# Kernel optimization log

Hardware: AMD Instinct MI355X
Metric: run time of the kernel (lower is better)

Reference implementation:

```python
import jax, jax.numpy as jnp
import numpy as np

DIM = 1024
NUM_HEADS = 16
HEAD_DIM = DIM // NUM_HEADS
EPS = 1e-6


def setup_inputs() -> dict:
    key = jax.random.key(0)
    ks = jax.random.split(key, 9)
    B, S = 4, 4096
    std = 1.0 / np.sqrt(DIM)
    inp = {
        "x": jax.random.normal(ks[0], (B, S, DIM), dtype=jnp.float32),
        "attention_mask": jnp.ones((B, S), dtype=jnp.float32),
        "Wq": jax.random.normal(ks[1], (DIM, DIM), dtype=jnp.float32) * std,
        "bq": jnp.zeros((DIM,), dtype=jnp.float32),
        "Wk": jax.random.normal(ks[2], (DIM, DIM), dtype=jnp.float32) * std,
        "bk": jnp.zeros((DIM,), dtype=jnp.float32),
        "Wv": jax.random.normal(ks[3], (DIM, DIM), dtype=jnp.float32) * std,
        "bv": jnp.zeros((DIM,), dtype=jnp.float32),
        "Wo": jax.random.normal(ks[4], (DIM, DIM), dtype=jnp.float32) * std,
        "bo": jnp.zeros((DIM,), dtype=jnp.float32),
    }
    return inp


def _phi(x):
    # ELU + 1 feature map (positive-valued kernel features)
    return jax.nn.elu(x) + 1.0


def reference(x, attention_mask, Wq, bq, Wk, bk, Wv, bv, Wo, bo):
    B, S, _ = x.shape
    H, D = NUM_HEADS, HEAD_DIM
    q = (x @ Wq.T + bq).reshape(B, S, H, D)
    k = (x @ Wk.T + bk).reshape(B, S, H, D)
    v = (x @ Wv.T + bv).reshape(B, S, H, D)
    q = _phi(q)
    k = _phi(k)
    m = attention_mask[:, :, None, None]
    k = k * m
    v = v * m
    # kv state: [B, H, D, D]
    kv = jnp.einsum("bshd,bshm->bhdm", k, v)
    qkv = jnp.einsum("bshd,bhdm->bshm", q, kv)
    k_sum = k.sum(axis=1)  # [B, H, D]
    normalizer = jnp.einsum("bshd,bhd->bsh", q, k_sum) + EPS
    out = (qkv / normalizer[..., None]).reshape(B, S, DIM)
    return out @ Wo.T + bo
```

## Files before the change

### kernel.cpp

```cpp
#include <hip/hip_runtime.h>

typedef unsigned short u16;
typedef float f32x4 __attribute__((ext_vector_type(4)));
typedef __bf16 bf16x8 __attribute__((ext_vector_type(8)));
typedef unsigned short us8 __attribute__((ext_vector_type(8)));

#define EPS_ 1e-6f

__device__ __forceinline__ u16 f2bf(float f) {
    unsigned u = __float_as_uint(f);
    u += 0x7FFFu + ((u >> 16) & 1u);
    return (u16)(u >> 16);
}
__device__ __forceinline__ float bf2f(u16 h) {
    return __uint_as_float(((unsigned)h) << 16);
}
__device__ __forceinline__ void gload_lds16(const void* g, void* l) {
    __builtin_amdgcn_global_load_lds(
        (const __attribute__((address_space(1))) void*)g,
        (__attribute__((address_space(3))) void*)l, 16, 0, 0);
}

__global__ __launch_bounds__(256) void f32_to_bf16_kernel(
    const float* __restrict__ src, u16* __restrict__ dst, int n4)
{
    int i = blockIdx.x * 256 + threadIdx.x;
    if (i >= n4) return;
    float4 f = ((const float4*)src)[i];
    ushort4 o;
    o.x = f2bf(f.x); o.y = f2bf(f.y); o.z = f2bf(f.z); o.w = f2bf(f.w);
    ((ushort4*)dst)[i] = o;
}


__device__ __forceinline__ void stage_half(
    const u16* __restrict__ src, int K, int kbase, char* slot, int tid)
{
    const int w = tid >> 6, l = tid & 63;
    #pragma unroll
    for (int j = 0; j < 2; ++j) {
        int c16 = j * 512 + w * 64 + l;
        int row = c16 >> 2;
        int sl  = c16 & 3;
        int ksrc = kbase + ((sl ^ ((row >> 1) & 3)) << 3);
        gload_lds16(src + (size_t)row * K + ksrc, slot + j * 8192 + w * 1024);
    }
}

#define BARRIER()  asm volatile("s_barrier" ::: "memory")
#define VMCNT8()   asm volatile("s_waitcnt vmcnt(8)" ::: "memory")
#define LGKM0()    asm volatile("s_waitcnt lgkmcnt(0)" ::: "memory")

#define LOADA(base, MOFF) \
    af0 = *(const bf16x8*)((base) + aoff + (MOFF) + 0);    \
    af1 = *(const bf16x8*)((base) + aoff + (MOFF) + 1024); \
    af2 = *(const bf16x8*)((base) + aoff + (MOFF) + 2048); \
    af3 = *(const bf16x8*)((base) + aoff + (MOFF) + 3072);

#define LOADB(base) \
    bf0 = *(const bf16x8*)((base) + boff + 0);    \
    bf1 = *(const bf16x8*)((base) + boff + 1024); \
    bf2 = *(const bf16x8*)((base) + boff + 2048); \
    bf3 = *(const bf16x8*)((base) + boff + 3072);

#define MFMA1(M_, N_, AF_, BF_) \
    acc[M_][N_] = __builtin_amdgcn_mfma_f32_16x16x32_bf16(BF_, AF_, acc[M_][N_], 0, 0, 0)

#define MFMA_BLOCK(M0) do { \
    MFMA1(M0+0, 0, af0, bf0); MFMA1(M0+0, 1, af0, bf1); MFMA1(M0+0, 2, af0, bf2); MFMA1(M0+0, 3, af0, bf3); \
    MFMA1(M0+1, 0, af1, bf0); MFMA1(M0+1, 1, af1, bf1); MFMA1(M0+1, 2, af1, bf2); MFMA1(M0+1, 3, af1, bf3); \
    MFMA1(M0+2, 0, af2, bf0); MFMA1(M0+2, 1, af2, bf1); MFMA1(M0+2, 2, af2, bf2); MFMA1(M0+2, 3, af2, bf3); \
    MFMA1(M0+3, 0, af3, bf0); MFMA1(M0+3, 1, af3, bf1); MFMA1(M0+3, 2, af3, bf2); MFMA1(M0+3, 3, af3, bf3); \
} while (0)

template<int MODE>
__global__ __launch_bounds__(512, 2) void gemm8p(
    const u16* __restrict__ A, const u16* __restrict__ B,
    const float* __restrict__ bias,
    u16* __restrict__ oq, u16* __restrict__ ok, u16* __restrict__ ov,
    float* __restrict__ outf, int M, int N, int K)
{
    extern __shared__ char lds[];
    const int tid  = threadIdx.x;
    const int lane = tid & 63;
    const int wv   = tid >> 6;
    const int wm   = wv >> 2;
    const int wn   = wv & 3;
    const int NT = K >> 6;

    int bx, by;
    {
        const int gx = gridDim.x;
        int wg  = blockIdx.y * gx + blockIdx.x;
        int cpx = (gx * gridDim.y) >> 3;
        int swz = (wg & 7) * cpx + (wg >> 3);
        bx = swz % gx; by = swz / gx;
    }

    const u16* Ab = A + (size_t)by * 256 * K;
    const u16* Bb = B + (size_t)bx * 256 * K;

    const int i  = lane & 15, g = lane >> 4;
    const int fo = ((g ^ ((i >> 1) & 3)) << 4);
    const int aoff = (wm * 128 + i) * 64 + fo;
    const int boff = (wn * 64 + i) * 64 + fo;

    f32x4 acc[8][4];
    #pragma unroll
    for (int m = 0; m < 8; ++m)
        #pragma unroll
        for (int n = 0; n < 4; ++n) {
            acc[m][n][0] = 0.f; acc[m][n][1] = 0.f;
            acc[m][n][2] = 0.f; acc[m][n][3] = 0.f;
        }

    stage_half(Ab, K, 0,  lds + 0,             tid);
    stage_half(Bb, K, 0,  lds + 16384,         tid);
    stage_half(Ab, K, 32, lds + 32768,         tid);
    stage_half(Bb, K, 32, lds + 49152,         tid);
    stage_half(Ab, K, 64, lds + 65536 + 0,     tid);
    stage_half(Bb, K, 64, lds + 65536 + 16384, tid);
    VMCNT8();
    BARRIER();

    for (int t = 0; t < NT; ++t) {
        char* cb = lds + ((t & 1) << 16);
        char* nb = lds + (((t + 1) & 1) << 16);
        const int t1 = (t + 1 < NT) ? t + 1 : NT - 1;
        const int t2 = (t + 2 < NT) ? t + 2 : NT - 1;
        const int k1src = t1 * 64 + 32;
        const int k2src = t2 * 64;

        bf16x8 af0, af1, af2, af3, bf0, bf1, bf2, bf3;

        LOADA(cb, 0);
        LOADB(cb + 16384);
        stage_half(Ab, K, k1src, nb + 32768, tid);
        BARRIER();
        LGKM0();
        __builtin_amdgcn_s_setprio(1);
        MFMA_BLOCK(0);
        __builtin_amdgcn_s_setprio(0);
        BARRIER();

        LOADA(cb, 4096);
        stage_half(Bb, K, k1src, nb + 49152, tid);
        VMCNT8();
        BARRIER();
        LGKM0();
        __builtin_amdgcn_s_setprio(1);
        MFMA_BLOCK(4);
        __builtin_amdgcn_s_setprio(0);
        BARRIER();

        LOADA(cb + 32768, 0);
        LOADB(cb + 49152);
        stage_half(Ab, K, k2src, cb + 0, tid);
        BARRIER();
        LGKM0();
        __builtin_amdgcn_s_setprio(1);
        MFMA_BLOCK(0);
        __builtin_amdgcn_s_setprio(0);
        BARRIER();

        LOADA(cb + 32768, 4096);
        stage_half(Bb, K, k2src, cb + 16384, tid);
        VMCNT8();
        BARRIER();
        LGKM0();
        __builtin_amdgcn_s_setprio(1);
        MFMA_BLOCK(4);
        __builtin_amdgcn_s_setprio(0);
        BARRIER();
    }
    asm volatile("s_waitcnt vmcnt(0)" ::: "memory");

    const int rowg0 = by * 256 + wm * 128;
    const int colg0 = bx * 256 + wn * 64;

    if (MODE == 1) {
        const int which = colg0 >> 10;
        u16* dst = (which == 0) ? oq : ((which == 1) ? ok : ov);
        const bool dophi = (which < 2);
        const int cbo = colg0 & 1023;
        float4 bs[4];
        #pragma unroll
        for (int n = 0; n < 4; ++n)
            bs[n] = *(const float4*)(bias + colg0 + n * 16 + g * 4);
        #pragma unroll
        for (int m = 0; m < 8; ++m) {
            int row = rowg0 + m * 16 + i;
            #pragma unroll
            for (int n = 0; n < 4; ++n) {
                float v0 = acc[m][n][0] + bs[n].x;
                float v1 = acc[m][n][1] + bs[n].y;
                float v2 = acc[m][n][2] + bs[n].z;
                float v3 = acc[m][n][3] + bs[n].w;
                if (dophi) {
                    v0 = (v0 > 0.f) ? (v0 + 1.f) : __expf(v0);
                    v1 = (v1 > 0.f) ? (v1 + 1.f) : __expf(v1);
                    v2 = (v2 > 0.f) ? (v2 + 1.f) : __expf(v2);
                    v3 = (v3 > 0.f) ? (v3 + 1.f) : __expf(v3);
                }
                ushort4 o;
                o.x = f2bf(v0); o.y = f2bf(v1); o.z = f2bf(v2); o.w = f2bf(v3);
                *(ushort4*)(dst + (size_t)row * 1024 + cbo + n * 16 + g * 4) = o;
            }
        }
    } else {
        float4 bs[4];
        #pragma unroll
        for (int n = 0; n < 4; ++n)
            bs[n] = *(const float4*)(bias + colg0 + n * 16 + g * 4);
        #pragma unroll
        for (int m = 0; m < 8; ++m) {
            int row = rowg0 + m * 16 + i;
            #pragma unroll
            for (int n = 0; n < 4; ++n) {
                float4 o;
                o.x = acc[m][n][0] + bs[n].x;
                o.y = acc[m][n][1] + bs[n].y;
                o.z = acc[m][n][2] + bs[n].z;
                o.w = acc[m][n][3] + bs[n].w;
                *(float4*)(outf + (size_t)row * N + colg0 + n * 16 + g * 4) = o;
            }
        }
    }
}

__global__ __launch_bounds__(256) void kv_partial(
    const u16* __restrict__ kbf, const u16* __restrict__ vbf,
    const float* __restrict__ mask, float* __restrict__ kvp, float* __restrict__ ksp)
{
    const int bh = blockIdx.x, ch = blockIdx.y;
    const int b = bh >> 4, h = bh & 15;
    const int tid = threadIdx.x;
    __shared__ __align__(16) float ks[32][64];
    __shared__ __align__(16) float vs[32][64];
    const int dg = tid >> 4, mg = tid & 15;
    float acc[4][4] = {};
    float ksa[4] = {};
    const int s0 = ch * 256;
    const int lr = tid >> 3, lc = (tid & 7) * 8;
    for (int sb = 0; sb < 256; sb += 32) {
        {
            size_t grow = (size_t)b * 4096 + (s0 + sb + lr);
            float mm = mask[grow];
            size_t off = (grow << 10) + (h << 6) + lc;
            us8 ku = __builtin_bit_cast(us8, *(const bf16x8*)(kbf + off));
            us8 vu = __builtin_bit_cast(us8, *(const bf16x8*)(vbf + off));
            #pragma unroll
            for (int j = 0; j < 8; ++j) {
                ks[lr][lc + j] = bf2f(ku[j]) * mm;
                vs[lr][lc + j] = bf2f(vu[j]) * mm;
            }
        }
        __syncthreads();
        #pragma unroll
        for (int ss = 0; ss < 32; ++ss) {
            float4 k4 = *(const float4*)&ks[ss][dg << 2];
            float4 v4 = *(const float4*)&vs[ss][mg << 2];
            float ka[4] = {k4.x, k4.y, k4.z, k4.w};
            float va[4] = {v4.x, v4.y, v4.z, v4.w};
            #pragma unroll
            for (int di = 0; di < 4; ++di) {
                ksa[di] += ka[di];
                #pragma unroll
                for (int mi = 0; mi < 4; ++mi) acc[di][mi] += ka[di] * va[mi];
            }
        }
        __syncthreads();
    }
    float* o = kvp + (((size_t)ch * 64 + bh) << 12);
    #pragma unroll
    for (int di = 0; di < 4; ++di)
        #pragma unroll
        for (int mi = 0; mi < 4; ++mi)
            o[(dg * 4 + di) * 64 + (mg * 4 + mi)] = acc[di][mi];
    if (mg == 0) {
        float* os = ksp + (((size_t)ch * 64 + bh) << 6);
        #pragma unroll
        for (int di = 0; di < 4; ++di) os[dg * 4 + di] = ksa[di];
    }
}

__global__ __launch_bounds__(256) void kv_reduce(
    const float* __restrict__ kvp, const float* __restrict__ ksp,
    u16* __restrict__ kvTbf, u16* __restrict__ ksumbf)
{
    const int bh = blockIdx.x, tid = threadIdx.x;
    for (int idx = tid; idx < 4096; idx += 256) {
        float s = 0.f;
        #pragma unroll
        for (int c = 0; c < 16; ++c) s += kvp[(((size_t)c * 64 + bh) << 12) + idx];
        int d = idx >> 6, m = idx & 63;
        kvTbf[((size_t)bh << 12) + (m << 6) + d] = f2bf(s);
    }
    if (tid < 64) {
        float s = 0.f;
        #pragma unroll
        for (int c = 0; c < 16; ++c) s += ksp[(((size_t)c * 64 + bh) << 6) + tid];
        ksumbf[(bh << 6) + tid] = f2bf(s);
    }
}

__global__ __launch_bounds__(256) void attn_kernel(
    const u16* __restrict__ qbf, const u16* __restrict__ kvTbf,
    const u16* __restrict__ ksumbf, u16* __restrict__ attnbf)
{
    const int bh = blockIdx.x;
    const int b = bh >> 4, h = bh & 15;
    const int tid = threadIdx.x, lane = tid & 63, wv = tid >> 6;
    __shared__ __align__(16) u16 kvs[64 * 64];
    __shared__ __align__(16) u16 kss[64];

    {
        const uint4* src = (const uint4*)(kvTbf + ((size_t)bh << 12));
        for (int u = tid; u < 512; u += 256) {
            uint4 d4 = src[u];
            int m = u >> 3, slot = u & 7;
            *(uint4*)((char*)kvs + m * 128 + ((slot ^ (m & 7)) << 4)) = d4;
        }
        if (tid < 32)
            ((unsigned*)kss)[tid] = ((const unsigned*)(ksumbf + ((size_t)bh << 6)))[tid];
    }
    __syncthreads();

    bf16x8 bfr[2][4], bnf[2];
    #pragma unroll
    for (int kk = 0; kk < 2; ++kk) {
        int kslot = kk * 4 + (lane >> 4);
        #pragma unroll
        for (int n = 0; n < 4; ++n) {
            int m = n * 16 + (lane & 15);
            bfr[kk][n] = *(const bf16x8*)((const char*)kvs + m * 128 +
                                          ((kslot ^ (m & 7)) << 4));
        }
        #pragma unroll
        for (int i2 = 0; i2 < 8; ++i2) bnf[kk][i2] = (__bf16)0.0f;
        if ((lane & 15) == 0)
            bnf[kk] = *(const bf16x8*)((const char*)kss + (kslot << 4));
    }

    const int sbase = blockIdx.y * 256 + wv * 16;
    for (int it = 0; it < 4; ++it) {
        const int st = sbase + it * 64;
        f32x4 acc[4], nacc;
        #pragma unroll
        for (int n = 0; n < 4; ++n) {
            acc[n][0] = 0.f; acc[n][1] = 0.f; acc[n][2] = 0.f; acc[n][3] = 0.f;
        }
        nacc[0] = 0.f; nacc[1] = 0.f; nacc[2] = 0.f; nacc[3] = 0.f;
        #pragma unroll
        for (int kk = 0; kk < 2; ++kk) {
            size_t goff = (((size_t)(b * 4096 + st + (lane & 15))) << 10) +
                          (h << 6) + kk * 32 + ((lane >> 4) << 3);
            bf16x8 af = *(const bf16x8*)(qbf + goff);
            #pragma unroll
            for (int n = 0; n < 4; ++n)
                acc[n] = __builtin_amdgcn_mfma_f32_16x16x32_bf16(af, bfr[kk][n], acc[n], 0, 0, 0);
            nacc = __builtin_amdgcn_mfma_f32_16x16x32_bf16(af, bnf[kk], nacc, 0, 0, 0);
        }
        float inv[4];
        #pragma unroll
        for (int j = 0; j < 4; ++j) {
            float nj = __shfl(nacc[j], lane & 48);
            inv[j] = 1.0f / (nj + EPS_);
        }
        #pragma unroll
        for (int n = 0; n < 4; ++n)
            #pragma unroll
            for (int j = 0; j < 4; ++j) {
                int row = st + ((lane >> 4) << 2) + j;
                attnbf[(((size_t)(b * 4096 + row)) << 10) + (h << 6) + n * 16 + (lane & 15)]
                    = f2bf(acc[n][j] * inv[j]);
            }
    }
}

extern "C" void kernel_launch(void* const* d_in, const int* in_sizes, int n_in,
                              void* d_out, int out_size, void* d_ws, size_t ws_size,
                              hipStream_t stream) {
    const float* x    = (const float*)d_in[0];
    const float* mask = (const float*)d_in[1];
    const float* Wq   = (const float*)d_in[2];
    const float* bq   = (const float*)d_in[3];
    const float* Wk   = (const float*)d_in[4];
    const float* bk   = (const float*)d_in[5];
    const float* Wv   = (const float*)d_in[6];
    const float* bv   = (const float*)d_in[7];
    const float* Wo   = (const float*)d_in[8];
    const float* bo   = (const float*)d_in[9];
    float* out = (float*)d_out;

    if (ws_size < 142606336u) return;

    char* ws = (char*)d_ws;
    u16*   xbf    = (u16*)ws;
    u16*   wqkvbf = (u16*)(ws + 33554432);
    float* bcat   = (float*)(ws + 39845888);
    u16*   qbf    = (u16*)(ws + 41943040);
    u16*   kbf    = qbf + 16777216;
    u16*   vbf    = kbf + 16777216;
    u16*   attnbf = kbf;
    float* kvp    = (float*)ws;
    float* ksp    = (float*)(ws + 16777216);
    u16*   kvTbf  = (u16*)(ws + 17039360);
    u16*   ksumbf = (u16*)(ws + 17563648);
    u16*   wobf   = (u16*)(ws + 20971520);

    f32_to_bf16_kernel<<<16384, 256, 0, stream>>>(x,  xbf,  16777216 / 4);
    f32_to_bf16_kernel<<<1024,  256, 0, stream>>>(Wq, wqkvbf,           1048576 / 4);
    f32_to_bf16_kernel<<<1024,  256, 0, stream>>>(Wk, wqkvbf + 1048576, 1048576 / 4);
    f32_to_bf16_kernel<<<1024,  256, 0, stream>>>(Wv, wqkvbf + 2097152, 1048576 / 4);
    hipMemcpyAsync(bcat,        bq, 4096, hipMemcpyDeviceToDevice, stream);
    hipMemcpyAsync(bcat + 1024, bk, 4096, hipMemcpyDeviceToDevice, stream);
    hipMemcpyAsync(bcat + 2048, bv, 4096, hipMemcpyDeviceToDevice, stream);

    gemm8p<1><<<dim3(12, 64), 512, 131072, stream>>>(
        xbf, wqkvbf, bcat, qbf, kbf, vbf, nullptr, 16384, 3072, 1024);

    f32_to_bf16_kernel<<<1024, 256, 0, stream>>>(Wo, wobf, 1048576 / 4);

    kv_partial<<<dim3(64, 16), 256, 0, stream>>>(kbf, vbf, mask, kvp, ksp);
    kv_reduce<<<64, 256, 0, stream>>>(kvp, ksp, kvTbf, ksumbf);

    attn_kernel<<<dim3(64, 16), 256, 0, stream>>>(qbf, kvTbf, ksumbf, attnbf);

    gemm8p<0><<<dim3(4, 64), 512, 131072, stream>>>(
        attnbf, wobf, bo, nullptr, nullptr, nullptr, out, 16384, 1024, 1024);
}
```

Baseline: 242.3 us.

## Restructure GEMM main loop into two half-steps with fewer barriers

The K-loop of the bf16 MFMA GEMM moves from four quarter-phases to two half-phases. Each phase loads all eight A fragments and four B fragments from LDS, then issues 32 MFMAs in one block. Both global-to-LDS stages for the next tile are issued together, and the loop now syncs with a single vmcnt(4) wait and two barriers per iteration instead of eight. The aim is to cut barrier and waitcnt stalls and give the scheduler longer MFMA runs. The cost is more live fragment registers and less fine-grained overlap between LDS reads and MFMAs.

```diff
diff --git a/kernel.cpp b/kernel.cpp
--- a/kernel.cpp
+++ b/kernel.cpp
@@ -48,16 +48,19 @@
 }
 
 #define BARRIER()  asm volatile("s_barrier" ::: "memory")
-#define VMCNT8()   asm volatile("s_waitcnt vmcnt(8)" ::: "memory")
-#define LGKM0()    asm volatile("s_waitcnt lgkmcnt(0)" ::: "memory")
-
-#define LOADA(base, MOFF) \
-    af0 = *(const bf16x8*)((base) + aoff + (MOFF) + 0);    \
-    af1 = *(const bf16x8*)((base) + aoff + (MOFF) + 1024); \
-    af2 = *(const bf16x8*)((base) + aoff + (MOFF) + 2048); \
-    af3 = *(const bf16x8*)((base) + aoff + (MOFF) + 3072);
-
-#define LOADB(base) \
+#define VMCNT4()   asm volatile("s_waitcnt vmcnt(4)" ::: "memory")
+
+#define LOADA8(base) \
+    af0 = *(const bf16x8*)((base) + aoff + 0);    \
+    af1 = *(const bf16x8*)((base) + aoff + 1024); \
+    af2 = *(const bf16x8*)((base) + aoff + 2048); \
+    af3 = *(const bf16x8*)((base) + aoff + 3072); \
+    af4 = *(const bf16x8*)((base) + aoff + 4096); \
+    af5 = *(const bf16x8*)((base) + aoff + 5120); \
+    af6 = *(const bf16x8*)((base) + aoff + 6144); \
+    af7 = *(const bf16x8*)((base) + aoff + 7168);
+
+#define LOADB4(base) \
     bf0 = *(const bf16x8*)((base) + boff + 0);    \
     bf1 = *(const bf16x8*)((base) + boff + 1024); \
     bf2 = *(const bf16x8*)((base) + boff + 2048); \
@@ -66,11 +69,15 @@
 #define MFMA1(M_, N_, AF_, BF_) \
     acc[M_][N_] = __builtin_amdgcn_mfma_f32_16x16x32_bf16(BF_, AF_, acc[M_][N_], 0, 0, 0)
 
-#define MFMA_BLOCK(M0) do { \
-    MFMA1(M0+0, 0, af0, bf0); MFMA1(M0+0, 1, af0, bf1); MFMA1(M0+0, 2, af0, bf2); MFMA1(M0+0, 3, af0, bf3); \
-    MFMA1(M0+1, 0, af1, bf0); MFMA1(M0+1, 1, af1, bf1); MFMA1(M0+1, 2, af1, bf2); MFMA1(M0+1, 3, af1, bf3); \
-    MFMA1(M0+2, 0, af2, bf0); MFMA1(M0+2, 1, af2, bf1); MFMA1(M0+2, 2, af2, bf2); MFMA1(M0+2, 3, af2, bf3); \
-    MFMA1(M0+3, 0, af3, bf0); MFMA1(M0+3, 1, af3, bf1); MFMA1(M0+3, 2, af3, bf2); MFMA1(M0+3, 3, af3, bf3); \
+#define MFMA_ROW(M_, AF_) \
+    MFMA1(M_, 0, AF_, bf0); MFMA1(M_, 1, AF_, bf1); \
+    MFMA1(M_, 2, AF_, bf2); MFMA1(M_, 3, AF_, bf3);
+
+#define MFMA_HALF() do { \
+    __builtin_amdgcn_s_setprio(1); \
+    MFMA_ROW(0, af0); MFMA_ROW(1, af1); MFMA_ROW(2, af2); MFMA_ROW(3, af3); \
+    MFMA_ROW(4, af4); MFMA_ROW(5, af5); MFMA_ROW(6, af6); MFMA_ROW(7, af7); \
+    __builtin_amdgcn_s_setprio(0); \
 } while (0)
 
 template<int MODE>
@@ -120,58 +127,33 @@
     stage_half(Bb, K, 32, lds + 49152,         tid);
     stage_half(Ab, K, 64, lds + 65536 + 0,     tid);
     stage_half(Bb, K, 64, lds + 65536 + 16384, tid);
-    VMCNT8();
-    BARRIER();
 
     for (int t = 0; t < NT; ++t) {
         char* cb = lds + ((t & 1) << 16);
         char* nb = lds + (((t + 1) & 1) << 16);
         const int t1 = (t + 1 < NT) ? t + 1 : NT - 1;
         const int t2 = (t + 2 < NT) ? t + 2 : NT - 1;
-        const int k1src = t1 * 64 + 32;
-        const int k2src = t2 * 64;
-
-        bf16x8 af0, af1, af2, af3, bf0, bf1, bf2, bf3;
-
-        LOADA(cb, 0);
-        LOADB(cb + 16384);
-        stage_half(Ab, K, k1src, nb + 32768, tid);
+
+        VMCNT4();
         BARRIER();
-        LGKM0();
-        __builtin_amdgcn_s_setprio(1);
-        MFMA_BLOCK(0);
-        __builtin_amdgcn_s_setprio(0);
+
+        bf16x8 af0, af1, af2, af3, af4, af5, af6, af7, bf0, bf1, bf2, bf3;
+
+        stage_half(Ab, K, t1 * 64 + 32, nb + 32768, tid);
+        stage_half(Bb, K, t1 * 64 + 32, nb + 49152, tid);
+
+        LOADA8(cb);
+        LOADB4(cb + 16384);
+        MFMA_HALF();
+
         BARRIER();
 
-        LOADA(cb, 4096);
-        stage_half(Bb, K, k1src, nb + 49152, tid);
-        VMCNT8();
-        BARRIER();
-        LGKM0();
-        __builtin_amdgcn_s_setprio(1);
-        MFMA_BLOCK(4);
-        __builtin_amdgcn_s_setprio(0);
-        BARRIER();
-
-        LOADA(cb + 32768, 0);
-        LOADB(cb + 49152);
-        stage_half(Ab, K, k2src, cb + 0, tid);
-        BARRIER();
-        LGKM0();
-        __builtin_amdgcn_s_setprio(1);
-        MFMA_BLOCK(0);
-        __builtin_amdgcn_s_setprio(0);
-        BARRIER();
-
-        LOADA(cb + 32768, 4096);
-        stage_half(Bb, K, k2src, cb + 16384, tid);
-        VMCNT8();
-        BARRIER();
-        LGKM0();
-        __builtin_amdgcn_s_setprio(1);
-        MFMA_BLOCK(4);
-        __builtin_amdgcn_s_setprio(0);
-        BARRIER();
+        stage_half(Ab, K, t2 * 64, cb + 0,     tid);
+        stage_half(Bb, K, t2 * 64, cb + 16384, tid);
+
+        LOADA8(cb + 32768);
+        LOADB4(cb + 49152);
+        MFMA_HALF();
     }
     asm volatile("s_waitcnt vmcnt(0)" ::: "memory");
 
```

Measured after the change: 247.2 us. 1.02x slower.
